# Kernel optimization log

Hardware: AMD Instinct MI355X
Metric: run time of the kernel (lower is better)

## Reference

```python
import jax, jax.numpy as jnp
import numpy as np

S, B, DIN, DBERT, H, L = 128, 32, 256, 768, 512, 2
NT_POS, NT_MORPH = 32, 64


def setup_inputs() -> dict:
    key = jax.random.key(0)
    ks = iter(jax.random.split(key, 32))
    def rn(shape, s=0.1):
        return jax.random.normal(next(ks), shape, dtype=jnp.float32) * s
    D0 = DIN + DBERT  # 1024 == 2*H, so per-layer LSTM weights stack cleanly
    return {
        "src_segments": rn((S, B, DIN), 1.0),
        "bert_encodings": rn((B, DBERT), 1.0),
        "labels_pos": jax.random.randint(next(ks), (S, B), 0, NT_POS, dtype=jnp.int32),
        "labels_morph": jax.random.randint(next(ks), (S, B), 0, NT_MORPH, dtype=jnp.int32),
        # stacked LSTM params: [layer, direction, ...], PyTorch gate order i,f,g,o
        "w_ih": rn((L, 2, 4 * H, D0)),
        "w_hh": rn((L, 2, 4 * H, H)),
        "b_ih": rn((L, 2, 4 * H)),
        "b_hh": rn((L, 2, 4 * H)),
        "head_w_pos": rn((NT_POS, 2 * H)),
        "head_b_pos": rn((NT_POS,)),
        "head_w_morph": rn((NT_MORPH, 2 * H)),
        "head_b_morph": rn((NT_MORPH,)),
        "start_pos": rn((NT_POS,)), "end_pos": rn((NT_POS,)), "trans_pos": rn((NT_POS, NT_POS)),
        "start_morph": rn((NT_MORPH,)), "end_morph": rn((NT_MORPH,)), "trans_morph": rn((NT_MORPH, NT_MORPH)),
    }


def _run_dir(x, w_ih, w_hh, b):
    # x: [S, B, D]; one LSTM direction via scan over time
    bsz, hd = x.shape[1], w_hh.shape[1]
    def step(carry, xt):
        h, c = carry
        g = xt @ w_ih.T + h @ w_hh.T + b  # [B, 4H]
        i, f, gg, o = jnp.split(g, 4, axis=-1)
        c = jax.nn.sigmoid(f) * c + jax.nn.sigmoid(i) * jnp.tanh(gg)
        h = jax.nn.sigmoid(o) * jnp.tanh(c)
        return (h, c), h
    init = (jnp.zeros((bsz, hd), x.dtype), jnp.zeros((bsz, hd), x.dtype))
    _, hs = jax.lax.scan(step, init, x)
    return hs


def _bilstm(x, w_ih, w_hh, b_ih, b_hh):
    out = x
    for l in range(w_ih.shape[0]):
        b = b_ih[l] + b_hh[l]
        fwd = _run_dir(out, w_ih[l, 0], w_hh[l, 0], b[0])
        bwd = _run_dir(out[::-1], w_ih[l, 1], w_hh[l, 1], b[1])[::-1]
        out = jnp.concatenate([fwd, bwd], axis=-1)  # [S, B, 2H]
    return out


def _crf_ll(em, tags, start, trans, end):
    # torchcrf log-likelihood, mask=None, reduction='sum'. em: [S,B,K], tags: [S,B]
    bsz = em.shape[1]
    first = start[tags[0]] + em[0, jnp.arange(bsz), tags[0]]
    em_sc = jnp.take_along_axis(em, tags[..., None], axis=2)[..., 0]  # [S,B]
    num = first + trans[tags[:-1], tags[1:]].sum(0) + em_sc[1:].sum(0) + end[tags[-1]]
    def step(alpha, et):  # alpha: [B,K]
        return jax.nn.logsumexp(alpha[:, :, None] + trans[None], axis=1) + et, None
    alpha, _ = jax.lax.scan(step, start[None, :] + em[0], em[1:])
    den = jax.nn.logsumexp(alpha + end[None, :], axis=1)
    return jnp.sum(num - den)


def reference(src_segments, bert_encodings, labels_pos, labels_morph,
              w_ih, w_hh, b_ih, b_hh,
              head_w_pos, head_b_pos, head_w_morph, head_b_morph,
              start_pos, end_pos, trans_pos, start_morph, end_morph, trans_morph):
    # bert encodings are repeated over seq and concatenated on features
    bert = jnp.broadcast_to(bert_encodings[None], (src_segments.shape[0],) + bert_encodings.shape)
    emb = jnp.concatenate([src_segments, bert], axis=-1)  # dropout p=0 -> identity
    out = _bilstm(emb, w_ih, w_hh, b_ih, b_hh)            # [S,B,2H]
    feat_pos = out @ head_w_pos.T + head_b_pos            # [S,B,32]
    feat_morph = out @ head_w_morph.T + head_b_morph      # [S,B,64]
    ll = (_crf_ll(feat_pos, labels_pos, start_pos, trans_pos, end_pos)
          + _crf_ll(feat_morph, labels_morph, start_morph, trans_morph, end_morph))
    return -ll  # loss = -sum_f crf_f(emissions_f, labels_f)
```

## Files before the change

### kernel.cpp

```cpp
#include <hip/hip_runtime.h>


typedef unsigned short u16;
typedef unsigned int u32;
typedef unsigned long long u64;
typedef __attribute__((ext_vector_type(8))) __bf16 bf16x8;
typedef __attribute__((ext_vector_type(4))) float floatx4;

static __device__ __forceinline__ u16 f2bf(float f) {
  u32 u = __float_as_uint(f);
  u += 0x7fffu + ((u >> 16) & 1u);
  return (u16)(u >> 16);
}
static __device__ __forceinline__ float bf2f(u32 bits) {
  return __uint_as_float(bits << 16);
}
static __device__ __forceinline__ float sigf(float x) {
  return 1.0f / (1.0f + __expf(-x));
}
static __device__ __forceinline__ float tanh_(float x) {
  return 1.0f - 2.0f / (1.0f + __expf(2.0f * x));
}
static __device__ __forceinline__ floatx4 mfma16(bf16x8 a, bf16x8 b, floatx4 c) {
  return __builtin_amdgcn_mfma_f32_16x16x32_bf16(a, b, c, 0, 0, 0);
}

__global__ __launch_bounds__(256) void prep_kernel(
    const float* __restrict__ w_ih, const float* __restrict__ w_hh,
    const float* __restrict__ b_ih, const float* __restrict__ b_hh,
    const float* __restrict__ src,  const float* __restrict__ bert,
    const float* __restrict__ hwp,  const float* __restrict__ hbp,
    const float* __restrict__ hwm,  const float* __restrict__ hbm,
    u16* __restrict__ Wsrc, u16* __restrict__ Wbert, u16* __restrict__ Wih1,
    u16* __restrict__ Whh,  u16* __restrict__ SrcBf, u16* __restrict__ BertBf,
    u16* __restrict__ Wheads, float* __restrict__ b0sum, float* __restrict__ b1sum,
    float* __restrict__ hb, float* __restrict__ dout)
{
  const int NA = 4194304;
  const int NB = 4194304;
  const int NC = 4194304;
  const int ND = 1048576;
  const int NE = 24576;
  const int NF = 98304;
  const int NG = 8192;
  const int NH = 96;
  const int TOTAL = NA + NB + NC + ND + NE + NF + NG + NH + 1;
  for (int i = blockIdx.x * 256 + threadIdx.x; i < TOTAL; i += gridDim.x * 256) {
    int x = i;
    if (x < NA) {
      int c = x & 1023, r = x >> 10;
      float v = w_ih[x];
      if (c < 256) Wsrc[r * 256 + c] = f2bf(v);
      else         Wbert[r * 768 + (c - 256)] = f2bf(v);
      continue;
    }
    x -= NA;
    if (x < NB) { Wih1[x] = f2bf(w_ih[NA + x]); continue; }
    x -= NB;
    if (x < NC) { Whh[x] = f2bf(w_hh[x]); continue; }
    x -= NC;
    if (x < ND) { SrcBf[x] = f2bf(src[x]); continue; }
    x -= ND;
    if (x < NE) { BertBf[x] = f2bf(bert[x]); continue; }
    x -= NE;
    if (x < NF) {
      Wheads[x] = f2bf(x < 32768 ? hwp[x] : hwm[x - 32768]);
      continue;
    }
    x -= NF;
    if (x < NG) {
      float v = b_ih[x] + b_hh[x];
      if (x < 4096) b0sum[x] = v; else b1sum[x - 4096] = v;
      continue;
    }
    x -= NG;
    if (x < NH) { hb[x] = (x < 32) ? hbp[x] : hbm[x - 32]; continue; }
    dout[0] = 0.f;
  }
}

__global__ __launch_bounds__(256) void gemm_nt(
    const u16* __restrict__ A, int lda,
    const u16* __restrict__ B, int ldb,
    float* __restrict__ C, int ldc,
    int M, int N, int K,
    const float* __restrict__ bias_n,
    const float* __restrict__ auxBN, int auxld,
    int mode)
{
  __shared__ __align__(16) u16 As[128 * 64];
  __shared__ __align__(16) u16 Bs[128 * 64];
  const int m0 = blockIdx.y * 128, n0 = blockIdx.x * 128;
  const int tid = threadIdx.x;
  const int wv = tid >> 6, ln = tid & 63;
  const int wm = wv & 1, wn = wv >> 1;
  const int q = ln >> 4, l15 = ln & 15;
  floatx4 acc[4][4];
#pragma unroll
  for (int a = 0; a < 4; ++a)
#pragma unroll
    for (int b2 = 0; b2 < 4; ++b2) acc[a][b2] = (floatx4){0.f, 0.f, 0.f, 0.f};

  for (int kk = 0; kk < K; kk += 64) {
    __syncthreads();
#pragma unroll
    for (int j = 0; j < 4; ++j) {
      const int idx = j * 256 + tid;
      const int r = idx >> 3, cc = idx & 7;
      const int slot = cc ^ (r & 7);
      const int ra = min(m0 + r, M - 1);
      *(int4*)&As[r * 64 + slot * 8] = *(const int4*)&A[(long)ra * lda + kk + cc * 8];
      const int rb = min(n0 + r, N - 1);
      *(int4*)&Bs[r * 64 + slot * 8] = *(const int4*)&B[(long)rb * ldb + kk + cc * 8];
    }
    __syncthreads();
#pragma unroll
    for (int ks = 0; ks < 2; ++ks) {
      bf16x8 af[4], bf[4];
#pragma unroll
      for (int im = 0; im < 4; ++im) {
        const int r = wm * 64 + im * 16 + l15;
        const int slot = (ks * 4 + q) ^ (r & 7);
        af[im] = *(const bf16x8*)&As[r * 64 + slot * 8];
      }
#pragma unroll
      for (int jn = 0; jn < 4; ++jn) {
        const int r = wn * 64 + jn * 16 + l15;
        const int slot = (ks * 4 + q) ^ (r & 7);
        bf[jn] = *(const bf16x8*)&Bs[r * 64 + slot * 8];
      }
#pragma unroll
      for (int im = 0; im < 4; ++im)
#pragma unroll
        for (int jn = 0; jn < 4; ++jn)
          acc[im][jn] = mfma16(af[im], bf[jn], acc[im][jn]);
    }
  }
  if (mode == 0) {
#pragma unroll
    for (int im = 0; im < 4; ++im)
#pragma unroll
      for (int jn = 0; jn < 4; ++jn) {
        const int n = n0 + wn * 64 + jn * 16 + l15;
        if (n < N) {
          const float badd = bias_n ? bias_n[n] : 0.f;
#pragma unroll
          for (int rg = 0; rg < 4; ++rg) {
            const int m = m0 + wm * 64 + im * 16 + q * 4 + rg;
            if (m < M) {
              float v = acc[im][jn][rg] + badd;
              if (auxBN) v += auxBN[(long)(m & 31) * auxld + n];
              C[(long)m * ldc + n] = v;
            }
          }
        }
      }
  } else {
    u64* G = (u64*)C;
#pragma unroll
    for (int im = 0; im < 4; ++im)
#pragma unroll
      for (int jn = 0; jn < 4; ++jn) {
        const int n = n0 + wn * 64 + jn * 16 + l15;
        const int dirsel = n >> 11, nn = n & 2047;
        const int gt = nn >> 9, u = nn & 511;
        const int ub = u >> 4, low = u & 15;
        const int wvl = low >> 2, jl = low & 3;
        const int l15l = gt * 4 + jl;
        const int m = m0 + wm * 64 + im * 16 + q * 4;
        const int s = m >> 5, b0 = m & 31;
        const int mh = b0 >> 4, qq = (b0 >> 2) & 3;
        const float badd = bias_n ? bias_n[n] : 0.f;
        u64 pk = 0;
#pragma unroll
        for (int rg = 0; rg < 4; ++rg) {
          float v = acc[im][jn][rg] + badd;
          if (auxBN) v += auxBN[(long)(b0 + rg) * auxld + n];
          pk |= (u64)f2bf(v) << (16 * rg);
        }
        G[(((((long)dirsel * 128 + s) * 2 + mh) * 32 + ub) * 4 + wvl) * 64
          + l15l * 4 + qq] = pk;
      }
  }
}

__global__ __launch_bounds__(256, 1) void lstm_rec(
    const u16* __restrict__ gates,
    u16* __restrict__ out,
    const u16* __restrict__ whh)
{
  __shared__ __align__(16) u16 h_lds[16 * 512];
  __shared__ float gsc[4][16][17];
  const int bid = blockIdx.x;
  const int dir = bid >> 6;
  const int mh = (bid >> 5) & 1;
  const int ub = bid & 31;
  const int u0 = ub * 16;
  const int tid = threadIdx.x;
  const int wv = tid >> 6;
  const int ln = tid & 63;
  const int q = ln >> 4, l15 = ln & 15;

  const int gate_r = (l15 >> 2) * 512 + u0 + wv * 4 + (l15 & 3);

  bf16x8 bfrag[16];
  {
    const u16* wp = whh + ((long)dir * 2048 + gate_r) * 512 + q * 8;
#pragma unroll
    for (int ks = 0; ks < 16; ++ks)
      bfrag[ks] = *(const bf16x8*)(wp + ks * 32);
  }

  float c = 0.f;
  const int b_glob = mh * 16 + l15;

  const u64* gbase = (const u64*)gates
      + ((((long)dir * 128 * 2 + mh) * 32 + ub) * 4 + wv) * 64 + l15 * 4 + q;

  u64 gcur = gbase[(long)(dir ? 127 : 0) * 16384];
  u64 gnext = 0;

  for (int t = 0; t < 128; ++t) {
    const int s = dir ? (127 - t) : t;
    if (t < 127) {
      const int sn = dir ? (126 - t) : (t + 1);
      gnext = gbase[(long)sn * 16384];
    }
    floatx4 acc = (floatx4){0.f, 0.f, 0.f, 0.f};
    if (t > 0) {
      const int sp = dir ? (s + 1) : (s - 1);
      const u64* ubp = (const u64*)(out + (((long)sp * 32 + mh * 16) * 1024 + (long)dir * 512));
      u64 v8[8];
#pragma unroll
      for (int j = 0; j < 8; ++j) {
        const int idx = j * 256 + tid;
        const int r = idx >> 7, c4 = idx & 127;
        v8[j] = __hip_atomic_load((u64*)(ubp + (long)r * 256 + c4),
                                  __ATOMIC_RELAXED, __HIP_MEMORY_SCOPE_AGENT);
      }
      while (true) {
        bool bad = false;
#pragma unroll
        for (int j = 0; j < 8; ++j) bad |= ((v8[j] & 0xffffULL) == 0xffffULL);
        if (!bad) break;
#pragma unroll
        for (int j = 0; j < 8; ++j) {
          if ((v8[j] & 0xffffULL) == 0xffffULL) {
            const int idx = j * 256 + tid;
            const int r = idx >> 7, c4 = idx & 127;
            v8[j] = __hip_atomic_load((u64*)(ubp + (long)r * 256 + c4),
                                      __ATOMIC_RELAXED, __HIP_MEMORY_SCOPE_AGENT);
          }
        }
      }
#pragma unroll
      for (int j = 0; j < 8; ++j) {
        const int idx = j * 256 + tid;
        const int r = idx >> 7, c4 = idx & 127;
        const int cc8 = c4 >> 1, hf = c4 & 1;
        *(u64*)&h_lds[r * 512 + ((cc8 ^ (r & 7)) << 3) + (hf << 2)] = v8[j];
      }
      __syncthreads();
      floatx4 acc1 = (floatx4){0.f, 0.f, 0.f, 0.f};
#pragma unroll
      for (int ks = 0; ks < 16; ks += 2) {
        const int slot0 = (ks * 4 + q) ^ (l15 & 7);
        bf16x8 a0 = *(const bf16x8*)&h_lds[l15 * 512 + slot0 * 8];
        acc = mfma16(a0, bfrag[ks], acc);
        const int slot1 = ((ks + 1) * 4 + q) ^ (l15 & 7);
        bf16x8 a1 = *(const bf16x8*)&h_lds[l15 * 512 + slot1 * 8];
        acc1 = mfma16(a1, bfrag[ks + 1], acc1);
      }
      acc += acc1;
    }
#pragma unroll
    for (int rg = 0; rg < 4; ++rg)
      gsc[wv][q * 4 + rg][l15] = acc[rg] + bf2f((u32)((gcur >> (16 * rg)) & 0xffffu));
    const float gi = gsc[wv][l15][q];
    const float gf = gsc[wv][l15][4 + q];
    const float gg = gsc[wv][l15][8 + q];
    const float go = gsc[wv][l15][12 + q];
    const float iv = sigf(gi), fv = sigf(gf), gv = tanh_(gg), ov = sigf(go);
    c = fv * c + iv * gv;
    const float h = ov * tanh_(c);
    const u32 hv = (u32)f2bf(h);
    const u32 p1 = (u32)__shfl_xor((int)hv, 16);
    const u32 lo32 = hv | (p1 << 16);
    const u64 w64 = (u64)lo32 |
                    ((u64)(u32)__shfl_xor((int)lo32, 32) << 32);
    if (q == 0)
      __hip_atomic_store(
          (u64*)&out[((long)s * 32 + b_glob) * 1024 + dir * 512 + u0 + wv * 4],
          w64, __ATOMIC_RELAXED, __HIP_MEMORY_SCOPE_AGENT);
    gcur = gnext;
  }
}

template <int K>
static __device__ void crf_body(const float* __restrict__ feat, int off,
                                const int* __restrict__ labels, int b,
                                const float* __restrict__ start,
                                const float* __restrict__ end_,
                                const float* __restrict__ trans,
                                float* __restrict__ outp,
                                float* transT, float (*alpha)[64],
                                float* red)
{
  const int tid = threadIdx.x;
  for (int i = tid; i < K * K; i += 256) {
    int kk = i / K, kp2 = i % K;
    transT[kp2 * 65 + kk] = trans[i];
  }
  if (tid < K) alpha[0][tid] = start[tid] + feat[b * 96 + off + tid];
  __syncthreads();
  constexpr int Kq = K / 4;
  const int kp = tid >> 2, k4 = tid & 3;
  const bool act = kp < K;
  int p = 0;
  for (int s = 1; s < 128; ++s) {
    float x[Kq];
    float mx = -3e38f;
    if (act) {
      const float* tr = &transT[kp * 65 + k4 * Kq];
      const float* al = &alpha[p][k4 * Kq];
#pragma unroll
      for (int i2 = 0; i2 < Kq; ++i2) { x[i2] = al[i2] + tr[i2]; mx = fmaxf(mx, x[i2]); }
    }
    mx = fmaxf(mx, __shfl_xor(mx, 1));
    mx = fmaxf(mx, __shfl_xor(mx, 2));
    float ss = 0.f;
    if (act) {
#pragma unroll
      for (int i2 = 0; i2 < Kq; ++i2) ss += __expf(x[i2] - mx);
    }
    ss += __shfl_xor(ss, 1);
    ss += __shfl_xor(ss, 2);
    if (act && k4 == 0)
      alpha[p ^ 1][kp] = mx + __logf(ss) + feat[(s * 32 + b) * 96 + off + kp];
    __syncthreads();
    p ^= 1;
  }
  if (tid < 128) {
    const int tg = labels[tid * 32 + b];
    float term = feat[(tid * 32 + b) * 96 + off + tg];
    if (tid == 0) term += start[tg];
    else          term += trans[labels[(tid - 1) * 32 + b] * K + tg];
    if (tid == 127) term += end_[tg];
    red[tid] = term;
  }
  __syncthreads();
  if (tid == 0) {
    float num = 0.f;
    for (int i = 0; i < 128; ++i) num += red[i];
    float mx = -3e38f;
    for (int k = 0; k < K; ++k) mx = fmaxf(mx, alpha[p][k] + end_[k]);
    float ss = 0.f;
    for (int k = 0; k < K; ++k) ss += __expf(alpha[p][k] + end_[k] - mx);
    const float den = mx + __logf(ss);
    atomicAdd(outp, den - num);
  }
}

__global__ __launch_bounds__(256) void crf_kernel(
    const float* __restrict__ feat,
    const int* __restrict__ labp, const int* __restrict__ labm,
    const float* __restrict__ stp, const float* __restrict__ enp, const float* __restrict__ trp,
    const float* __restrict__ stm, const float* __restrict__ enm, const float* __restrict__ trm,
    float* __restrict__ outp)
{
  __shared__ float transT[64 * 65];
  __shared__ float alpha[2][64];
  __shared__ float red[128];
  const int task = blockIdx.x >> 5, b = blockIdx.x & 31;
  if (task == 0) crf_body<32>(feat, 0,  labp, b, stp, enp, trp, outp, transT, alpha, red);
  else           crf_body<64>(feat, 32, labm, b, stm, enm, trm, outp, transT, alpha, red);
}

extern "C" void kernel_launch(void* const* d_in, const int* in_sizes, int n_in,
                              void* d_out, int out_size, void* d_ws, size_t ws_size,
                              hipStream_t stream) {
  const float* src  = (const float*)d_in[0];
  const float* bert = (const float*)d_in[1];
  const int*   labp = (const int*)d_in[2];
  const int*   labm = (const int*)d_in[3];
  const float* w_ih = (const float*)d_in[4];
  const float* w_hh = (const float*)d_in[5];
  const float* b_ih = (const float*)d_in[6];
  const float* b_hh = (const float*)d_in[7];
  const float* hwp  = (const float*)d_in[8];
  const float* hbp  = (const float*)d_in[9];
  const float* hwm  = (const float*)d_in[10];
  const float* hbm  = (const float*)d_in[11];
  const float* stp  = (const float*)d_in[12];
  const float* enp  = (const float*)d_in[13];
  const float* trp  = (const float*)d_in[14];
  const float* stm  = (const float*)d_in[15];
  const float* enm  = (const float*)d_in[16];
  const float* trm  = (const float*)d_in[17];

  char* ws = (char*)d_ws;
  u16*   Wsrc     = (u16*)(ws + 0);
  u16*   Wbert    = (u16*)(ws + 2097152);
  u16*   Wih1     = (u16*)(ws + 8388608);
  u16*   Whh      = (u16*)(ws + 16777216);
  u16*   SrcBf    = (u16*)(ws + 25165824);
  u16*   BertBf   = (u16*)(ws + 27262976);
  u16*   Wheads   = (u16*)(ws + 27312128);
  float* b0sum    = (float*)(ws + 27508736);
  float* b1sum    = (float*)(ws + 27525120);
  float* hb       = (float*)(ws + 27541504);
  float* bertpart = (float*)(ws + 27542272);
  float* feat     = (float*)(ws + 28066560);
  u16*   out0     = (u16*)(ws + 29639424);
  u16*   out1     = (u16*)(ws + 38028032);
  u16*   gates    = (u16*)(ws + 46416640);
  float* dout     = (float*)d_out;

  hipMemsetAsync(out0, 0xFF, 8388608, stream);
  hipMemsetAsync(out1, 0xFF, 8388608, stream);

  hipLaunchKernelGGL(prep_kernel, dim3(2048), dim3(256), 0, stream,
      w_ih, w_hh, b_ih, b_hh, src, bert, hwp, hbp, hwm, hbm,
      Wsrc, Wbert, Wih1, Whh, SrcBf, BertBf, Wheads, b0sum, b1sum, hb, dout);

  hipLaunchKernelGGL(gemm_nt, dim3(32, 1), dim3(256), 0, stream,
      BertBf, 768, Wbert, 768, bertpart, 4096, 32, 4096, 768,
      b0sum, (const float*)nullptr, 0, 0);

  hipLaunchKernelGGL(gemm_nt, dim3(32, 32), dim3(256), 0, stream,
      SrcBf, 256, Wsrc, 256, (float*)gates, 0, 4096, 4096, 256,
      (const float*)nullptr, bertpart, 4096, 1);

  {
    const u16* g = gates; u16* o = out0; const u16* wh = Whh;
    void* args[] = {&g, &o, &wh};
    hipLaunchCooperativeKernel(reinterpret_cast<void*>(&lstm_rec),
                               dim3(128), dim3(256), args, 0, stream);
  }

  hipLaunchKernelGGL(gemm_nt, dim3(32, 32), dim3(256), 0, stream,
      out0, 1024, Wih1, 1024, (float*)gates, 0, 4096, 4096, 1024,
      b1sum, (const float*)nullptr, 0, 1);

  {
    const u16* g = gates; u16* o = out1; const u16* wh = Whh + 2L * 2048 * 512;
    void* args[] = {&g, &o, &wh};
    hipLaunchCooperativeKernel(reinterpret_cast<void*>(&lstm_rec),
                               dim3(128), dim3(256), args, 0, stream);
  }

  hipLaunchKernelGGL(gemm_nt, dim3(1, 32), dim3(256), 0, stream,
      out1, 1024, Wheads, 1024, feat, 96, 4096, 96, 1024,
      hb, (const float*)nullptr, 0, 0);

  hipLaunchKernelGGL(crf_kernel, dim3(64), dim3(256), 0, stream,
      feat, labp, labm, stp, enp, trp, stm, enm, trm, dout);
}
```

Before: 894.2 us.

## Fuse LSTM input projection into recurrent kernel, dropping gate GEMMs

Each recurrent block now keeps its slice of W_ih in registers next to W_hh. Every step it stages the next timestep's input rows in LDS and computes the input-gate contribution with MFMAs, instead of reading a precomputed gates tensor. This removes the separate gate GEMMs, the bert partial-product GEMM and the gate buffer round-trip through memory. In exchange the serial per-step path gets extra MFMA work and global loads, and register pressure rises sharply. The prep kernel now builds a full concatenated bf16 embedding that repeats bert for every timestep, and the recurrent kernel is launched as an ordinary launch rather than a cooperative one.

```diff
diff --git a/kernel.cpp b/kernel.cpp
--- a/kernel.cpp
+++ b/kernel.cpp
@@ -12,9 +12,6 @@
   u += 0x7fffu + ((u >> 16) & 1u);
   return (u16)(u >> 16);
 }
-static __device__ __forceinline__ float bf2f(u32 bits) {
-  return __uint_as_float(bits << 16);
-}
 static __device__ __forceinline__ float sigf(float x) {
   return 1.0f / (1.0f + __expf(-x));
 }
@@ -29,52 +26,43 @@
     const float* __restrict__ w_ih, const float* __restrict__ w_hh,
     const float* __restrict__ b_ih, const float* __restrict__ b_hh,
     const float* __restrict__ src,  const float* __restrict__ bert,
-    const float* __restrict__ hwp,  const float* __restrict__ hbp,
-    const float* __restrict__ hwm,  const float* __restrict__ hbm,
-    u16* __restrict__ Wsrc, u16* __restrict__ Wbert, u16* __restrict__ Wih1,
-    u16* __restrict__ Whh,  u16* __restrict__ SrcBf, u16* __restrict__ BertBf,
-    u16* __restrict__ Wheads, float* __restrict__ b0sum, float* __restrict__ b1sum,
-    float* __restrict__ hb, float* __restrict__ dout)
+    const float* __restrict__ hwp,  const float* __restrict__ hwm,
+    const float* __restrict__ hbp,  const float* __restrict__ hbm,
+    u16* __restrict__ Wih, u16* __restrict__ Whh, u16* __restrict__ emb,
+    u16* __restrict__ Wheads, float* __restrict__ bsum, float* __restrict__ hb,
+    float* __restrict__ dout)
 {
-  const int NA = 4194304;
+  const int NA = 8388608;
   const int NB = 4194304;
-  const int NC = 4194304;
-  const int ND = 1048576;
-  const int NE = 24576;
-  const int NF = 98304;
-  const int NG = 8192;
-  const int NH = 96;
-  const int TOTAL = NA + NB + NC + ND + NE + NF + NG + NH + 1;
+  const int NC = 1048576;
+  const int ND = 3145728;
+  const int NE = 98304;
+  const int NF = 8192;
+  const int NG = 96;
+  const int TOTAL = NA + NB + NC + ND + NE + NF + NG + 1;
   for (int i = blockIdx.x * 256 + threadIdx.x; i < TOTAL; i += gridDim.x * 256) {
     int x = i;
-    if (x < NA) {
-      int c = x & 1023, r = x >> 10;
-      float v = w_ih[x];
-      if (c < 256) Wsrc[r * 256 + c] = f2bf(v);
-      else         Wbert[r * 768 + (c - 256)] = f2bf(v);
+    if (x < NA) { Wih[x] = f2bf(w_ih[x]); continue; }
+    x -= NA;
+    if (x < NB) { Whh[x] = f2bf(w_hh[x]); continue; }
+    x -= NB;
+    if (x < NC) {
+      const int row = x >> 8, c = x & 255;
+      emb[row * 1024 + c] = f2bf(src[x]);
       continue;
     }
-    x -= NA;
-    if (x < NB) { Wih1[x] = f2bf(w_ih[NA + x]); continue; }
-    x -= NB;
-    if (x < NC) { Whh[x] = f2bf(w_hh[x]); continue; }
     x -= NC;
-    if (x < ND) { SrcBf[x] = f2bf(src[x]); continue; }
+    if (x < ND) {
+      const int sb = x / 768, c = x - sb * 768;
+      emb[sb * 1024 + 256 + c] = f2bf(bert[(sb & 31) * 768 + c]);
+      continue;
+    }
     x -= ND;
-    if (x < NE) { BertBf[x] = f2bf(bert[x]); continue; }
+    if (x < NE) { Wheads[x] = f2bf(x < 32768 ? hwp[x] : hwm[x - 32768]); continue; }
     x -= NE;
-    if (x < NF) {
-      Wheads[x] = f2bf(x < 32768 ? hwp[x] : hwm[x - 32768]);
-      continue;
-    }
+    if (x < NF) { bsum[x] = b_ih[x] + b_hh[x]; continue; }
     x -= NF;
-    if (x < NG) {
-      float v = b_ih[x] + b_hh[x];
-      if (x < 4096) b0sum[x] = v; else b1sum[x - 4096] = v;
-      continue;
-    }
-    x -= NG;
-    if (x < NH) { hb[x] = (x < 32) ? hbp[x] : hbm[x - 32]; continue; }
+    if (x < NG) { hb[x] = (x < 32) ? hbp[x] : hbm[x - 32]; continue; }
     dout[0] = 0.f;
   }
 }
@@ -84,9 +72,7 @@
     const u16* __restrict__ B, int ldb,
     float* __restrict__ C, int ldc,
     int M, int N, int K,
-    const float* __restrict__ bias_n,
-    const float* __restrict__ auxBN, int auxld,
-    int mode)
+    const float* __restrict__ bias_n)
 {
   __shared__ __align__(16) u16 As[128 * 64];
   __shared__ __align__(16) u16 Bs[128 * 64];
@@ -136,59 +122,30 @@
           acc[im][jn] = mfma16(af[im], bf[jn], acc[im][jn]);
     }
   }
-  if (mode == 0) {
-#pragma unroll
-    for (int im = 0; im < 4; ++im)
-#pragma unroll
-      for (int jn = 0; jn < 4; ++jn) {
-        const int n = n0 + wn * 64 + jn * 16 + l15;
-        if (n < N) {
-          const float badd = bias_n ? bias_n[n] : 0.f;
-#pragma unroll
-          for (int rg = 0; rg < 4; ++rg) {
-            const int m = m0 + wm * 64 + im * 16 + q * 4 + rg;
-            if (m < M) {
-              float v = acc[im][jn][rg] + badd;
-              if (auxBN) v += auxBN[(long)(m & 31) * auxld + n];
-              C[(long)m * ldc + n] = v;
-            }
-          }
+#pragma unroll
+  for (int im = 0; im < 4; ++im)
+#pragma unroll
+    for (int jn = 0; jn < 4; ++jn) {
+      const int n = n0 + wn * 64 + jn * 16 + l15;
+      if (n < N) {
+        const float badd = bias_n ? bias_n[n] : 0.f;
+#pragma unroll
+        for (int rg = 0; rg < 4; ++rg) {
+          const int m = m0 + wm * 64 + im * 16 + q * 4 + rg;
+          if (m < M) C[(long)m * ldc + n] = acc[im][jn][rg] + badd;
         }
       }
-  } else {
-    u64* G = (u64*)C;
-#pragma unroll
-    for (int im = 0; im < 4; ++im)
-#pragma unroll
-      for (int jn = 0; jn < 4; ++jn) {
-        const int n = n0 + wn * 64 + jn * 16 + l15;
-        const int dirsel = n >> 11, nn = n & 2047;
-        const int gt = nn >> 9, u = nn & 511;
-        const int ub = u >> 4, low = u & 15;
-        const int wvl = low >> 2, jl = low & 3;
-        const int l15l = gt * 4 + jl;
-        const int m = m0 + wm * 64 + im * 16 + q * 4;
-        const int s = m >> 5, b0 = m & 31;
-        const int mh = b0 >> 4, qq = (b0 >> 2) & 3;
-        const float badd = bias_n ? bias_n[n] : 0.f;
-        u64 pk = 0;
-#pragma unroll
-        for (int rg = 0; rg < 4; ++rg) {
-          float v = acc[im][jn][rg] + badd;
-          if (auxBN) v += auxBN[(long)(b0 + rg) * auxld + n];
-          pk |= (u64)f2bf(v) << (16 * rg);
-        }
-        G[(((((long)dirsel * 128 + s) * 2 + mh) * 32 + ub) * 4 + wvl) * 64
-          + l15l * 4 + qq] = pk;
-      }
-  }
+    }
 }
 
 __global__ __launch_bounds__(256, 1) void lstm_rec(
-    const u16* __restrict__ gates,
+    const u16* __restrict__ xbuf,
     u16* __restrict__ out,
-    const u16* __restrict__ whh)
+    const u16* __restrict__ wih,
+    const u16* __restrict__ whh,
+    const float* __restrict__ bsum)
 {
+  __shared__ __align__(16) u16 x_lds[16 * 1024];
   __shared__ __align__(16) u16 h_lds[16 * 512];
   __shared__ float gsc[4][16][17];
   const int bid = blockIdx.x;
@@ -203,34 +160,67 @@
 
   const int gate_r = (l15 >> 2) * 512 + u0 + wv * 4 + (l15 & 3);
 
-  bf16x8 bfrag[16];
+  bf16x8 bh[16];
   {
     const u16* wp = whh + ((long)dir * 2048 + gate_r) * 512 + q * 8;
 #pragma unroll
-    for (int ks = 0; ks < 16; ++ks)
-      bfrag[ks] = *(const bf16x8*)(wp + ks * 32);
-  }
+    for (int ks = 0; ks < 16; ++ks) bh[ks] = *(const bf16x8*)(wp + ks * 32);
+  }
+  bf16x8 bx[32];
+  {
+    const u16* wp = wih + ((long)dir * 2048 + gate_r) * 1024 + q * 8;
+#pragma unroll
+    for (int ks = 0; ks < 32; ++ks) bx[ks] = *(const bf16x8*)(wp + ks * 32);
+  }
+  const float bias_r = bsum[dir * 2048 + gate_r];
 
   float c = 0.f;
   const int b_glob = mh * 16 + l15;
 
-  const u64* gbase = (const u64*)gates
-      + ((((long)dir * 128 * 2 + mh) * 32 + ub) * 4 + wv) * 64 + l15 * 4 + q;
-
-  u64 gcur = gbase[(long)(dir ? 127 : 0) * 16384];
-  u64 gnext = 0;
+  floatx4 gin;
+  {
+    const int s0 = dir ? 127 : 0;
+    const u64* xp = (const u64*)(xbuf + ((long)s0 * 32 + mh * 16) * 1024);
+#pragma unroll
+    for (int j = 0; j < 16; ++j) {
+      const int idx = j * 256 + tid;
+      const u64 v = xp[idx];
+      const int r = idx >> 8, c4 = idx & 255;
+      const int cc8 = c4 >> 1, hf = c4 & 1;
+      const int slot = (cc8 & ~7) | ((cc8 & 7) ^ (r & 7));
+      *(u64*)&x_lds[r * 1024 + slot * 8 + hf * 4] = v;
+    }
+    __syncthreads();
+    floatx4 gx0 = (floatx4){bias_r, bias_r, bias_r, bias_r};
+    floatx4 gx1 = (floatx4){0.f, 0.f, 0.f, 0.f};
+#pragma unroll
+    for (int ks = 0; ks < 32; ks += 2) {
+      const int c0 = ks * 4 + q;
+      const int slot0 = (c0 & ~7) | ((c0 & 7) ^ (l15 & 7));
+      bf16x8 a0 = *(const bf16x8*)&x_lds[l15 * 1024 + slot0 * 8];
+      gx0 = mfma16(a0, bx[ks], gx0);
+      const int c1 = (ks + 1) * 4 + q;
+      const int slot1 = (c1 & ~7) | ((c1 & 7) ^ (l15 & 7));
+      bf16x8 a1 = *(const bf16x8*)&x_lds[l15 * 1024 + slot1 * 8];
+      gx1 = mfma16(a1, bx[ks + 1], gx1);
+    }
+    gin = gx0 + gx1;
+    __syncthreads();
+  }
 
   for (int t = 0; t < 128; ++t) {
     const int s = dir ? (127 - t) : t;
+    u64 xv[16];
     if (t < 127) {
       const int sn = dir ? (126 - t) : (t + 1);
-      gnext = gbase[(long)sn * 16384];
-    }
-    floatx4 acc = (floatx4){0.f, 0.f, 0.f, 0.f};
+      const u64* xp = (const u64*)(xbuf + ((long)sn * 32 + mh * 16) * 1024);
+#pragma unroll
+      for (int j = 0; j < 16; ++j) xv[j] = xp[j * 256 + tid];
+    }
+    u64 v8[8];
     if (t > 0) {
       const int sp = dir ? (s + 1) : (s - 1);
       const u64* ubp = (const u64*)(out + (((long)sp * 32 + mh * 16) * 1024 + (long)dir * 512));
-      u64 v8[8];
 #pragma unroll
       for (int j = 0; j < 8; ++j) {
         const int idx = j * 256 + tid;
@@ -253,6 +243,18 @@
           }
         }
       }
+    }
+    if (t < 127) {
+#pragma unroll
+      for (int j = 0; j < 16; ++j) {
+        const int idx = j * 256 + tid;
+        const int r = idx >> 8, c4 = idx & 255;
+        const int cc8 = c4 >> 1, hf = c4 & 1;
+        const int slot = (cc8 & ~7) | ((cc8 & 7) ^ (r & 7));
+        *(u64*)&x_lds[r * 1024 + slot * 8 + hf * 4] = xv[j];
+      }
+    }
+    if (t > 0) {
 #pragma unroll
       for (int j = 0; j < 8; ++j) {
         const int idx = j * 256 + tid;
@@ -260,22 +262,40 @@
         const int cc8 = c4 >> 1, hf = c4 & 1;
         *(u64*)&h_lds[r * 512 + ((cc8 ^ (r & 7)) << 3) + (hf << 2)] = v8[j];
       }
-      __syncthreads();
+    }
+    __syncthreads();
+    floatx4 acc = (floatx4){0.f, 0.f, 0.f, 0.f};
+    if (t > 0) {
       floatx4 acc1 = (floatx4){0.f, 0.f, 0.f, 0.f};
 #pragma unroll
       for (int ks = 0; ks < 16; ks += 2) {
         const int slot0 = (ks * 4 + q) ^ (l15 & 7);
         bf16x8 a0 = *(const bf16x8*)&h_lds[l15 * 512 + slot0 * 8];
-        acc = mfma16(a0, bfrag[ks], acc);
+        acc = mfma16(a0, bh[ks], acc);
         const int slot1 = ((ks + 1) * 4 + q) ^ (l15 & 7);
         bf16x8 a1 = *(const bf16x8*)&h_lds[l15 * 512 + slot1 * 8];
-        acc1 = mfma16(a1, bfrag[ks + 1], acc1);
+        acc1 = mfma16(a1, bh[ks + 1], acc1);
       }
       acc += acc1;
     }
+    floatx4 gx0 = (floatx4){bias_r, bias_r, bias_r, bias_r};
+    floatx4 gx1 = (floatx4){0.f, 0.f, 0.f, 0.f};
+    if (t < 127) {
+#pragma unroll
+      for (int ks = 0; ks < 32; ks += 2) {
+        const int c0 = ks * 4 + q;
+        const int slot0 = (c0 & ~7) | ((c0 & 7) ^ (l15 & 7));
+        bf16x8 a0 = *(const bf16x8*)&x_lds[l15 * 1024 + slot0 * 8];
+        gx0 = mfma16(a0, bx[ks], gx0);
+        const int c1 = (ks + 1) * 4 + q;
+        const int slot1 = (c1 & ~7) | ((c1 & 7) ^ (l15 & 7));
+        bf16x8 a1 = *(const bf16x8*)&x_lds[l15 * 1024 + slot1 * 8];
+        gx1 = mfma16(a1, bx[ks + 1], gx1);
+      }
+    }
 #pragma unroll
     for (int rg = 0; rg < 4; ++rg)
-      gsc[wv][q * 4 + rg][l15] = acc[rg] + bf2f((u32)((gcur >> (16 * rg)) & 0xffffu));
+      gsc[wv][q * 4 + rg][l15] = acc[rg] + gin[rg];
     const float gi = gsc[wv][l15][q];
     const float gf = gsc[wv][l15][4 + q];
     const float gg = gsc[wv][l15][8 + q];
@@ -286,13 +306,12 @@
     const u32 hv = (u32)f2bf(h);
     const u32 p1 = (u32)__shfl_xor((int)hv, 16);
     const u32 lo32 = hv | (p1 << 16);
-    const u64 w64 = (u64)lo32 |
-                    ((u64)(u32)__shfl_xor((int)lo32, 32) << 32);
+    const u64 w64 = (u64)lo32 | ((u64)(u32)__shfl_xor((int)lo32, 32) << 32);
     if (q == 0)
       __hip_atomic_store(
           (u64*)&out[((long)s * 32 + b_glob) * 1024 + dir * 512 + u0 + wv * 4],
           w64, __ATOMIC_RELAXED, __HIP_MEMORY_SCOPE_AGENT);
-    gcur = gnext;
+    gin = gx0 + gx1;
   }
 }
 
@@ -399,59 +418,32 @@
   const float* trm  = (const float*)d_in[17];
 
   char* ws = (char*)d_ws;
-  u16*   Wsrc     = (u16*)(ws + 0);
-  u16*   Wbert    = (u16*)(ws + 2097152);
-  u16*   Wih1     = (u16*)(ws + 8388608);
-  u16*   Whh      = (u16*)(ws + 16777216);
-  u16*   SrcBf    = (u16*)(ws + 25165824);
-  u16*   BertBf   = (u16*)(ws + 27262976);
-  u16*   Wheads   = (u16*)(ws + 27312128);
-  float* b0sum    = (float*)(ws + 27508736);
-  float* b1sum    = (float*)(ws + 27525120);
-  float* hb       = (float*)(ws + 27541504);
-  float* bertpart = (float*)(ws + 27542272);
-  float* feat     = (float*)(ws + 28066560);
-  u16*   out0     = (u16*)(ws + 29639424);
-  u16*   out1     = (u16*)(ws + 38028032);
-  u16*   gates    = (u16*)(ws + 46416640);
-  float* dout     = (float*)d_out;
+  u16*   Wih    = (u16*)(ws + 0);
+  u16*   Whh    = (u16*)(ws + 16777216);
+  u16*   emb    = (u16*)(ws + 25165824);
+  u16*   Wheads = (u16*)(ws + 33554432);
+  float* bsum   = (float*)(ws + 33751040);
+  float* hb     = (float*)(ws + 33783808);
+  float* feat   = (float*)(ws + 33784320);
+  u16*   out0   = (u16*)(ws + 35357184);
+  u16*   out1   = (u16*)(ws + 43745792);
+  float* dout   = (float*)d_out;
 
   hipMemsetAsync(out0, 0xFF, 8388608, stream);
   hipMemsetAsync(out1, 0xFF, 8388608, stream);
 
   hipLaunchKernelGGL(prep_kernel, dim3(2048), dim3(256), 0, stream,
-      w_ih, w_hh, b_ih, b_hh, src, bert, hwp, hbp, hwm, hbm,
-      Wsrc, Wbert, Wih1, Whh, SrcBf, BertBf, Wheads, b0sum, b1sum, hb, dout);
-
-  hipLaunchKernelGGL(gemm_nt, dim3(32, 1), dim3(256), 0, stream,
-      BertBf, 768, Wbert, 768, bertpart, 4096, 32, 4096, 768,
-      b0sum, (const float*)nullptr, 0, 0);
-
-  hipLaunchKernelGGL(gemm_nt, dim3(32, 32), dim3(256), 0, stream,
-      SrcBf, 256, Wsrc, 256, (float*)gates, 0, 4096, 4096, 256,
-      (const float*)nullptr, bertpart, 4096, 1);
-
-  {
-    const u16* g = gates; u16* o = out0; const u16* wh = Whh;
-    void* args[] = {&g, &o, &wh};
-    hipLaunchCooperativeKernel(reinterpret_cast<void*>(&lstm_rec),
-                               dim3(128), dim3(256), args, 0, stream);
-  }
-
-  hipLaunchKernelGGL(gemm_nt, dim3(32, 32), dim3(256), 0, stream,
-      out0, 1024, Wih1, 1024, (float*)gates, 0, 4096, 4096, 1024,
-      b1sum, (const float*)nullptr, 0, 1);
-
-  {
-    const u16* g = gates; u16* o = out1; const u16* wh = Whh + 2L * 2048 * 512;
-    void* args[] = {&g, &o, &wh};
-    hipLaunchCooperativeKernel(reinterpret_cast<void*>(&lstm_rec),
-                               dim3(128), dim3(256), args, 0, stream);
-  }
+      w_ih, w_hh, b_ih, b_hh, src, bert, hwp, hwm, hbp, hbm,
+      Wih, Whh, emb, Wheads, bsum, hb, dout);
+
+  hipLaunchKernelGGL(lstm_rec, dim3(128), dim3(256), 0, stream,
+      emb, out0, Wih, Whh, bsum);
+
+  hipLaunchKernelGGL(lstm_rec, dim3(128), dim3(256), 0, stream,
+      out0, out1, Wih + 4194304, Whh + 2097152, bsum + 4096);
 
   hipLaunchKernelGGL(gemm_nt, dim3(1, 32), dim3(256), 0, stream,
-      out1, 1024, Wheads, 1024, feat, 96, 4096, 96, 1024,
-      hb, (const float*)nullptr, 0, 0);
+      out1, 1024, Wheads, 1024, feat, 96, 4096, 96, 1024, hb);
 
   hipLaunchKernelGGL(crf_kernel, dim3(64), dim3(256), 0, stream,
       feat, labp, labm, stp, enp, trp, stm, enm, trm, dout);
```

Measured after the change: 1.119 ms. 1.25x slower.
